# Kernel tuning notes

Hardware: AMD Instinct MI355X
Metric: run time of the kernel (lower is better)

Reference implementation:

```python
import jax, jax.numpy as jnp
import numpy as np

B, H, S, D = 2, 16, 2048, 64  # batch, heads, seq_len, depth (F_hidden)
EPS_ADJ = 1e-09
NEG_INF = -1000000000.0


def iswiglu(x):
    # x * silu(x) == x^2 * sigmoid(x), always >= 0
    return x * jax.nn.silu(x)


def setup_inputs() -> dict:
    key = jax.random.key(0)
    ks = jax.random.split(key, 8)
    Hin = jax.random.normal(ks[0], (B, H, S, D), jnp.float32)
    Hk = jax.random.normal(ks[1], (B, H, S, D), jnp.float32)
    Hv = jax.random.normal(ks[2], (B, H, S, D), jnp.float32)
    A = jax.random.normal(ks[3], (B, H, D, D), jnp.float32)
    # causal (look-ahead) mask: 1 where attention is disallowed
    mask = jnp.triu(jnp.ones((S, S), jnp.float32), k=1)[None, None, :, :]
    xavier = np.sqrt(2.0 / (D + D)).astype(np.float32)  # xavier_normal gain=1 for [D,D] fans
    W = jax.random.normal(ks[4], (H, D, D), jnp.float32) * xavier
    pw = jax.random.normal(ks[5], (H, D, D), jnp.float32) * xavier
    a = jax.random.normal(ks[6], (H, D, D), jnp.float32) * xavier
    b = jnp.zeros((H, D, D), jnp.float32)
    ba = jnp.zeros((H, D, D), jnp.float32)
    return {"Hin": Hin, "Hk": Hk, "Hv": Hv, "A": A, "mask": mask,
            "W": W, "b": b, "pw": pw, "a": a, "ba": ba}


def reference(Hin, Hk, Hv, A, mask, W, b, pw, a, ba):
    # metric-tensor transform: AW = iSwiGLU(W @ A + b) + eps   [B,H,D,D]
    x = jnp.einsum('hij,bhjk->bhik', W, A) + b[None]
    AW = iswiglu(x) + EPS_ADJ
    # energy-curvature tensor: avAp = a @ AW**pw + ba           [B,H,D,D]
    Ap = jnp.power(AW, pw[None])
    avAp = jnp.einsum('hij,bhjk->bhik', a, Ap) + ba[None]
    # bilinear attention scores: (Hin @ avAp) @ Hk^T / sqrt(D)  [B,H,S,S]
    q = jnp.matmul(Hin, avAp)
    Ep = jnp.matmul(q, jnp.swapaxes(Hk, -1, -2)) / jnp.sqrt(jnp.float32(D))
    E = jax.nn.softmax(Ep + mask * NEG_INF, axis=-1)
    Hout = jnp.matmul(E, Hv)                                   # [B,H,S,D]
    return Hout
```

## Files before the change

kernel.cpp:

```cpp
#include <hip/hip_runtime.h>


typedef short v8s __attribute__((ext_vector_type(8)));
typedef float v4f __attribute__((ext_vector_type(4)));

__device__ __forceinline__ float bf2f(unsigned short u) {
    union { unsigned int i; float f; } v; v.i = ((unsigned int)u) << 16; return v.f;
}
__device__ __forceinline__ unsigned short f2bf(float f) {
    unsigned int u = __float_as_uint(f);
    u += 0x7fffu + ((u >> 16) & 1u);
    return (unsigned short)(u >> 16);
}
__device__ __forceinline__ v4f mfma16(v8s a, v8s b, v4f c) {
    return __builtin_amdgcn_mfma_f32_16x16x32_bf16(a, b, c, 0, 0, 0);
}
__device__ __forceinline__ void gload_lds16(const void* g, void* l) {
    __builtin_amdgcn_global_load_lds(
        (const __attribute__((address_space(1))) void*)g,
        (__attribute__((address_space(3))) void*)l, 16, 0, 0);
}
__device__ __forceinline__ void block_sync() {
    asm volatile("" ::: "memory");
    __builtin_amdgcn_s_barrier();
    asm volatile("" ::: "memory");
}
__device__ __forceinline__ float fexp2(float x) {
    float r;
    asm volatile("v_exp_f32 %0, %1" : "=v"(r) : "v"(x));
    return r;
}

__global__ __launch_bounds__(256)
void pre1_kernel(const float* __restrict__ A,  const float* __restrict__ W,
                 const float* __restrict__ b,  const float* __restrict__ pw,
                 float* __restrict__ Pbuf)
{
    __shared__ float sA[4096], sW[512];
    const int bx = blockIdx.x, bh = blockIdx.y, h = bh & 15, t = threadIdx.x;
    const int lcol = t & 63, lrow = t >> 6, r0 = bx * 8;
    for (int i = t; i < 4096; i += 256) sA[i] = A[bh*4096 + i];
    for (int i = t; i < 512;  i += 256) sW[i] = W[h*4096 + r0*64 + i];
    __syncthreads();
    double acc[2];
    #pragma unroll
    for (int e = 0; e < 2; ++e)
        acc[e] = (double)b[h*4096 + (r0 + lrow + 4*e)*64 + lcol];
    #pragma unroll 4
    for (int jj = 0; jj < 16; ++jj) {
        double a0 = (double)sA[(4*jj+0)*64 + lcol];
        double a1 = (double)sA[(4*jj+1)*64 + lcol];
        double a2 = (double)sA[(4*jj+2)*64 + lcol];
        double a3 = (double)sA[(4*jj+3)*64 + lcol];
        #pragma unroll
        for (int e = 0; e < 2; ++e) {
            const float* wr = &sW[(lrow + 4*e)*64 + 4*jj];
            acc[e] += (double)wr[0]*a0 + (double)wr[1]*a1
                    + (double)wr[2]*a2 + (double)wr[3]*a3;
        }
    }
    #pragma unroll
    for (int e = 0; e < 2; ++e) {
        int idx = (r0 + lrow + 4*e)*64 + lcol;
        double v = acc[e];
        double sig = 1.0 / (1.0 + exp(-v));
        Pbuf[bh*4096 + idx] = (float)pow(v*v*sig + 1e-9, (double)pw[h*4096 + idx]);
    }
}

__global__ __launch_bounds__(256)
void pre2_kernel(const float* __restrict__ a,  const float* __restrict__ ba,
                 const float* __restrict__ Pbuf, float* __restrict__ avap)
{
    __shared__ float sP[4096], sa[512];
    const int bx = blockIdx.x, bh = blockIdx.y, h = bh & 15, t = threadIdx.x;
    const int lcol = t & 63, lrow = t >> 6, r0 = bx * 8;
    for (int i = t; i < 4096; i += 256) sP[i] = Pbuf[bh*4096 + i];
    for (int i = t; i < 512;  i += 256) sa[i] = a[h*4096 + r0*64 + i];
    __syncthreads();
    double acc[2];
    #pragma unroll
    for (int e = 0; e < 2; ++e)
        acc[e] = (double)ba[h*4096 + (r0 + lrow + 4*e)*64 + lcol];
    #pragma unroll 4
    for (int jj = 0; jj < 16; ++jj) {
        double a0 = (double)sP[(4*jj+0)*64 + lcol];
        double a1 = (double)sP[(4*jj+1)*64 + lcol];
        double a2 = (double)sP[(4*jj+2)*64 + lcol];
        double a3 = (double)sP[(4*jj+3)*64 + lcol];
        #pragma unroll
        for (int e = 0; e < 2; ++e) {
            const float* wr = &sa[(lrow + 4*e)*64 + 4*jj];
            acc[e] += (double)wr[0]*a0 + (double)wr[1]*a1
                    + (double)wr[2]*a2 + (double)wr[3]*a3;
        }
    }
    #pragma unroll
    for (int e = 0; e < 2; ++e)
        avap[bh*4096 + (r0 + lrow + 4*e)*64 + lcol] = (float)acc[e];
}

__global__ __launch_bounds__(256)
void pre_legacy(const float* __restrict__ A,  const float* __restrict__ W,
                const float* __restrict__ b,  const float* __restrict__ pw,
                const float* __restrict__ a,  const float* __restrict__ ba,
                float* __restrict__ avap)
{
    __shared__ float sW[4096], sA[4096], sP[4096];
    const int bh = blockIdx.x, h = bh & 15, t = threadIdx.x;
    const int lcol = t & 63, lrow = t >> 6;
    for (int i = t; i < 4096; i += 256) { sW[i] = W[h*4096+i]; sA[i] = A[bh*4096+i]; }
    __syncthreads();
    {
        double acc[16];
        #pragma unroll
        for (int e = 0; e < 16; ++e)
            acc[e] = (double)b[h*4096 + (lrow + 4*e)*64 + lcol];
        #pragma unroll 4
        for (int jj = 0; jj < 16; ++jj) {
            double a0 = (double)sA[(4*jj+0)*64 + lcol];
            double a1 = (double)sA[(4*jj+1)*64 + lcol];
            double a2 = (double)sA[(4*jj+2)*64 + lcol];
            double a3 = (double)sA[(4*jj+3)*64 + lcol];
            #pragma unroll
            for (int e = 0; e < 16; ++e) {
                const float* wr = &sW[(lrow + 4*e)*64 + 4*jj];
                acc[e] += (double)wr[0]*a0 + (double)wr[1]*a1
                        + (double)wr[2]*a2 + (double)wr[3]*a3;
            }
        }
        #pragma unroll
        for (int e = 0; e < 16; ++e) {
            int idx = (lrow + 4*e)*64 + lcol;
            double v = acc[e];
            double sig = 1.0 / (1.0 + exp(-v));
            sP[idx] = (float)pow(v*v*sig + 1e-9, (double)pw[h*4096 + idx]);
        }
    }
    __syncthreads();
    for (int i = t; i < 4096; i += 256) sW[i] = a[h*4096+i];
    __syncthreads();
    {
        double acc[16];
        #pragma unroll
        for (int e = 0; e < 16; ++e)
            acc[e] = (double)ba[h*4096 + (lrow + 4*e)*64 + lcol];
        #pragma unroll 4
        for (int jj = 0; jj < 16; ++jj) {
            double a0 = (double)sP[(4*jj+0)*64 + lcol];
            double a1 = (double)sP[(4*jj+1)*64 + lcol];
            double a2 = (double)sP[(4*jj+2)*64 + lcol];
            double a3 = (double)sP[(4*jj+3)*64 + lcol];
            #pragma unroll
            for (int e = 0; e < 16; ++e) {
                const float* wr = &sW[(lrow + 4*e)*64 + 4*jj];
                acc[e] += (double)wr[0]*a0 + (double)wr[1]*a1
                        + (double)wr[2]*a2 + (double)wr[3]*a3;
            }
        }
        #pragma unroll
        for (int e = 0; e < 16; ++e)
            avap[bh*4096 + (lrow + 4*e)*64 + lcol] = (float)acc[e];
    }
}

__global__ __launch_bounds__(256)
void q_kernel(const float* __restrict__ Hin, const float* __restrict__ avap,
              float* __restrict__ qout)
{
    __shared__ float sH[4096], sAv[4096];
    const int qt = blockIdx.x, bh = blockIdx.y, t = threadIdx.x;
    const int lcol = t & 63, lrow = t >> 6;
    const int base = bh*131072 + qt*4096;
    for (int i = t; i < 4096; i += 256) { sH[i] = Hin[base+i]; sAv[i] = avap[bh*4096+i]; }
    __syncthreads();
    float acc[16];
    #pragma unroll
    for (int e = 0; e < 16; ++e) acc[e] = 0.0f;
    #pragma unroll 4
    for (int jj = 0; jj < 16; ++jj) {
        float a0 = sAv[(4*jj+0)*64 + lcol];
        float a1 = sAv[(4*jj+1)*64 + lcol];
        float a2 = sAv[(4*jj+2)*64 + lcol];
        float a3 = sAv[(4*jj+3)*64 + lcol];
        #pragma unroll
        for (int e = 0; e < 16; ++e) {
            const float* hr = &sH[(lrow + 4*e)*64 + 4*jj];
            acc[e] += hr[0]*a0 + hr[1]*a1 + hr[2]*a2 + hr[3]*a3;
        }
    }
    #pragma unroll
    for (int e = 0; e < 16; ++e)
        qout[base + (lrow + 4*e)*64 + lcol] = acc[e] * 0.125f;
}

__global__ __launch_bounds__(256)
void kvprep_kernel(const float* __restrict__ Hk, const float* __restrict__ Hv,
                   unsigned short* __restrict__ kv)
{
    __shared__ float sV[4096];
    const int kt = blockIdx.x, bh = blockIdx.y, t = threadIdx.x;
    const float* hk = Hk + bh*131072 + kt*4096;
    const float* hv = Hv + bh*131072 + kt*4096;
    unsigned short* dst = kv + (size_t)(bh*32 + kt) * 12288;

    #pragma unroll
    for (int it = 0; it < 2; ++it) {
        int item = t + 256*it;
        int kr = item >> 3, oc = item & 7;
        const float* src = hk + kr*64 + oc*8;
        float4 g0 = *(const float4*)(src);
        float4 g1 = *(const float4*)(src + 4);
        float fv[8] = {g0.x,g0.y,g0.z,g0.w,g1.x,g1.y,g1.z,g1.w};
        v8s hi, lo;
        #pragma unroll
        for (int j = 0; j < 8; ++j) {
            unsigned short h = f2bf(fv[j]);
            hi[j] = (short)h;
            lo[j] = (short)f2bf(fv[j] - bf2f(h));
        }
        int addr = kr*64 + ((oc ^ (kr & 7)) << 3);
        *(v8s*)(dst + addr) = hi;
        *(v8s*)(dst + 4096 + addr) = lo;
    }
    #pragma unroll
    for (int i = 0; i < 4; ++i) {
        int idx = t + 256*i;
        int kr = idx >> 4, d0 = (idx & 15) * 4;
        float4 g = *(const float4*)(hv + kr*64 + d0);
        float gv[4] = {g.x, g.y, g.z, g.w};
        #pragma unroll
        for (int j = 0; j < 4; ++j)
            sV[kr*64 + ((d0 + j + kr) & 63)] = gv[j];
    }
    __syncthreads();
    #pragma unroll
    for (int it = 0; it < 2; ++it) {
        int item = t + 256*it;
        int d = item >> 3, oc = item & 7;
        v8s o;
        #pragma unroll
        for (int j = 0; j < 8; ++j) {
            int kr = oc*8 + j;
            o[j] = (short)f2bf(sV[kr*64 + ((d + kr) & 63)]);
        }
        *(v8s*)(dst + 8192 + d*64 + ((oc ^ (d & 7)) << 3)) = o;
    }
}

#define TILE_HW 12288
#define PBASE   24576
#define QLO     8192
#define AVT     16384

__global__ __launch_bounds__(512, 4)
void attn_kernel(const unsigned short* __restrict__ kv,
                 const float* __restrict__ Hin,
                 const float* __restrict__ avap,
                 float* __restrict__ io)
{
    __shared__ __align__(16) unsigned short sm16[32768];
    const int t    = threadIdx.x;
    const int w    = t >> 6;
    const int wq   = w & 3;
    const int lane = t & 63;
    const int l15  = lane & 15;
    const int quad = lane >> 4;
    const int g    = (blockIdx.x & 7) * 64 + (blockIdx.x >> 3);
    const int bh   = g >> 4;
    const int x    = g & 15;
    const int bhb  = bh * 131072;
    const int qt_a = x, qt_b = 31 - x;
    const int qsel = (w < 4) ? qt_a : qt_b;
    const int q0   = qsel * 64;
    const char* kvb = (const char*)(kv + (size_t)bh * 32 * TILE_HW);
    const int sl   = (quad ^ (l15 & 7)) << 3;
    const int wrow0 = (w < 4) ? wq*16 : 64 + wq*16;

    #pragma unroll
    for (int i = 0; i < 16; ++i) {
        int p = t + 512*i;
        int r = p >> 6, c = p & 63;
        int grow = (r < 64) ? (qt_a*64 + r) : (qt_b*64 + (r - 64));
        float v = Hin[bhb + grow*64 + c];
        unsigned short h = f2bf(v);
        int ad = r*64 + ((((c >> 3) ^ (r & 7)) << 3) | (c & 7));
        sm16[ad] = h;
        sm16[QLO + ad] = f2bf(v - bf2f(h));
    }
    #pragma unroll
    for (int i = 0; i < 8; ++i) {
        int p = t + 512*i;
        int k = p >> 6, n = p & 63;
        float v = avap[bh*4096 + p];
        unsigned short h = f2bf(v);
        int ad = n*64 + ((((k >> 3) ^ (n & 7)) << 3) | (k & 7));
        sm16[AVT + ad] = h;
        sm16[AVT + 4096 + ad] = f2bf(v - bf2f(h));
    }
    asm volatile("s_waitcnt lgkmcnt(0)" ::: "memory");
    block_sync();

    v4f qacc[4];
    {
        const int aoff = (wrow0 + l15)*64 + sl;
        v8s ahi0 = *(const v8s*)&sm16[aoff];
        v8s ahi1 = *(const v8s*)&sm16[aoff ^ 32];
        v8s alo0 = *(const v8s*)&sm16[QLO + aoff];
        v8s alo1 = *(const v8s*)&sm16[QLO + (aoff ^ 32)];
        #pragma unroll
        for (int nt = 0; nt < 4; ++nt) {
            const int bo = (16*nt + l15)*64 + sl;
            v8s bhi0 = *(const v8s*)&sm16[AVT + bo];
            v8s bhi1 = *(const v8s*)&sm16[AVT + (bo ^ 32)];
            v8s blo0 = *(const v8s*)&sm16[AVT + 4096 + bo];
            v8s blo1 = *(const v8s*)&sm16[AVT + 4096 + (bo ^ 32)];
            v4f acc = (v4f){0,0,0,0};
            acc = mfma16(alo0, bhi0, acc);
            acc = mfma16(alo1, bhi1, acc);
            acc = mfma16(ahi0, blo0, acc);
            acc = mfma16(ahi1, blo1, acc);
            acc = mfma16(ahi0, bhi0, acc);
            acc = mfma16(ahi1, bhi1, acc);
            qacc[nt] = acc;
        }
    }
    #pragma unroll
    for (int nt = 0; nt < 4; ++nt)
        #pragma unroll
        for (int reg = 0; reg < 4; ++reg) {
            float v = qacc[nt][reg] * 0.1803368801111244f;
            int row = wrow0 + quad*4 + reg;
            int col = 16*nt + l15;
            int ad = row*64 + ((((col >> 3) ^ (row & 7)) << 3) | (col & 7));
            unsigned short h = f2bf(v);
            sm16[ad] = h;
            sm16[QLO + ad] = f2bf(v - bf2f(h));
        }
    asm volatile("s_waitcnt lgkmcnt(0)" ::: "memory");
    v8s qhi[2], qlo[2];
    {
        const int aoff = (wrow0 + l15)*64 + sl;
        qhi[0] = *(const v8s*)&sm16[aoff];
        qhi[1] = *(const v8s*)&sm16[aoff ^ 32];
        qlo[0] = *(const v8s*)&sm16[QLO + aoff];
        qlo[1] = *(const v8s*)&sm16[QLO + (aoff ^ 32)];
    }
    asm volatile("s_waitcnt lgkmcnt(0)" ::: "memory");
    block_sync();

    #pragma unroll
    for (int j = 0; j < 3; ++j) {
        int c = 3*w + j;
        gload_lds16(kvb + c*1024 + (size_t)lane*16, (char*)sm16 + c*1024);
    }

    v4f O[4];
    float m_[4], l_[4];
    #pragma unroll
    for (int i = 0; i < 4; ++i) { O[i] = (v4f){0,0,0,0}; m_[i] = -1e30f; l_[i] = 0.0f; }

    for (int kt = 0; kt <= qt_b; ++kt) {
        const int base = (kt & 1) * TILE_HW;
        if (kt < qt_b) {
            const char* gs = kvb + (size_t)(kt+1) * (TILE_HW*2);
            char* lb = (char*)sm16 + ((kt+1) & 1) * (TILE_HW*2);
            #pragma unroll
            for (int j = 0; j < 3; ++j) {
                int c = 3*w + j;
                gload_lds16(gs + c*1024 + (size_t)lane*16, lb + c*1024);
            }
            asm volatile("s_waitcnt vmcnt(3)" ::: "memory");
        } else {
            asm volatile("s_waitcnt vmcnt(0)" ::: "memory");
        }
        block_sync();

        if (kt <= qsel) {
            v4f s[4];
            #pragma unroll
            for (int ct = 0; ct < 4; ++ct) {
                const int kb = base + (16*ct + l15)*64 + sl;
                v8s kh0 = *(const v8s*)&sm16[kb];
                v8s kh1 = *(const v8s*)&sm16[kb ^ 32];
                v8s kl0 = *(const v8s*)&sm16[kb + 4096];
                v8s kl1 = *(const v8s*)&sm16[(kb ^ 32) + 4096];
                v4f a = (v4f){0,0,0,0};
                a = mfma16(qlo[0], kh0, a);
                a = mfma16(qlo[1], kh1, a);
                a = mfma16(qhi[0], kl0, a);
                a = mfma16(qhi[1], kl1, a);
                a = mfma16(qhi[0], kh0, a);
                a = mfma16(qhi[1], kh1, a);
                s[ct] = a;
            }

            if (kt == qsel) {
                #pragma unroll
                for (int ct = 0; ct < 4; ++ct)
                    #pragma unroll
                    for (int r = 0; r < 4; ++r)
                        if (16*ct + l15 > 16*wq + quad*4 + r) s[ct][r] = -1e30f;
            }

            float pv[4][4];
            #pragma unroll
            for (int reg = 0; reg < 4; ++reg) {
                float rm = fmaxf(fmaxf(s[0][reg], s[1][reg]), fmaxf(s[2][reg], s[3][reg]));
                rm = fmaxf(rm, __shfl_xor(rm, 1));
                rm = fmaxf(rm, __shfl_xor(rm, 2));
                rm = fmaxf(rm, __shfl_xor(rm, 4));
                rm = fmaxf(rm, __shfl_xor(rm, 8));
                float mn = fmaxf(m_[reg], rm);
                float al = fexp2(m_[reg] - mn);
                m_[reg] = mn;
                float rs = 0.0f;
                #pragma unroll
                for (int ct = 0; ct < 4; ++ct) {
                    float e = fexp2(s[ct][reg] - mn);
                    pv[ct][reg] = e; rs += e;
                }
                rs += __shfl_xor(rs, 1);
                rs += __shfl_xor(rs, 2);
                rs += __shfl_xor(rs, 4);
                rs += __shfl_xor(rs, 8);
                l_[reg] = l_[reg]*al + rs;
                #pragma unroll
                for (int d = 0; d < 4; ++d) O[d][reg] *= al;
            }

            #pragma unroll
            for (int reg = 0; reg < 4; ++reg) {
                const int row = quad*4 + reg;
                #pragma unroll
                for (int ct = 0; ct < 4; ++ct)
                    sm16[PBASE + w*1024 + row*64 +
                         ((((2*ct + (l15 >> 3)) ^ (row & 7)) << 3) | (l15 & 7))]
                        = f2bf(pv[ct][reg]);
            }
            asm volatile("s_waitcnt lgkmcnt(0)" ::: "memory");

            const int pb = PBASE + w*1024 + l15*64 + sl;
            v8s pA0 = *(const v8s*)&sm16[pb];
            v8s pA1 = *(const v8s*)&sm16[pb ^ 32];
            #pragma unroll
            for (int d = 0; d < 4; ++d) {
                const int vb = base + 8192 + (16*d + l15)*64 + sl;
                v8s v0 = *(const v8s*)&sm16[vb];
                v8s v1 = *(const v8s*)&sm16[vb ^ 32];
                O[d] = mfma16(pA0, v0, O[d]);
                O[d] = mfma16(pA1, v1, O[d]);
            }
        }
        asm volatile("s_waitcnt lgkmcnt(0)" ::: "memory");
        block_sync();
    }

    #pragma unroll
    for (int reg = 0; reg < 4; ++reg) {
        float inv = 1.0f / l_[reg];
        int row = q0 + 16*wq + quad*4 + reg;
        #pragma unroll
        for (int d = 0; d < 4; ++d)
            io[bhb + row*64 + 16*d + l15] = O[d][reg] * inv;
    }
}

#define KHI 0
#define KLO 4608
#define VTB 9216
#define PB  13824

__global__ __launch_bounds__(256, 4)
void attn_legacy(const float* __restrict__ Hk, const float* __restrict__ Hv,
                 float* __restrict__ io)
{
    __shared__ __align__(16) unsigned short sm16[18432];
    const int t    = threadIdx.x;
    const int w    = t >> 6;
    const int lane = t & 63;
    const int l15  = lane & 15;
    const int quad = lane >> 4;
    const int x    = blockIdx.x;
    const int bh   = blockIdx.y;
    const int bhb  = bh * 131072;

    for (int pass = 0; pass < 2; ++pass) {
        const int qt = pass ? (31 - x) : x;
        const int q0 = qt * 64;

        v8s qhi[2], qlo[2];
        {
            const float* qr = io + bhb + (q0 + 16*w + l15)*64 + quad*8;
            #pragma unroll
            for (int ks = 0; ks < 2; ++ks)
                #pragma unroll
                for (int j = 0; j < 8; ++j) {
                    float qv = qr[32*ks + j];
                    unsigned short h = f2bf(qv);
                    unsigned short l = f2bf(qv - bf2f(h));
                    qhi[ks][j] = (short)h; qlo[ks][j] = (short)l;
                }
        }

        v4f O[4];
        float m_[4], l_[4];
        #pragma unroll
        for (int i = 0; i < 4; ++i) { O[i] = (v4f){0,0,0,0}; m_[i] = -1e30f; l_[i] = 0.0f; }

        for (int kt = 0; kt <= qt; ++kt) {
            __syncthreads();
            const int tb = bhb + kt*4096;
            #pragma unroll 4
            for (int i = 0; i < 16; ++i) {
                int p = t + 256*i;
                int kr = p >> 6, d = p & 63;
                float kvv = Hk[tb + p];
                unsigned short h = f2bf(kvv);
                sm16[KHI + kr*72 + d] = h;
                sm16[KLO + kr*72 + d] = f2bf(kvv - bf2f(h));
                sm16[VTB + d*72 + kr] = f2bf(Hv[tb + p]);
            }
            __syncthreads();

            v4f s[4];
            #pragma unroll
            for (int ct = 0; ct < 4; ++ct) {
                const unsigned short* kb = &sm16[(16*ct + l15)*72 + quad*8];
                v8s kh0 = *(const v8s*)(kb + KHI);
                v8s kh1 = *(const v8s*)(kb + KHI + 32);
                v8s kl0 = *(const v8s*)(kb + KLO);
                v8s kl1 = *(const v8s*)(kb + KLO + 32);
                v4f a = (v4f){0,0,0,0};
                a = mfma16(qlo[0], kh0, a);
                a = mfma16(qlo[1], kh1, a);
                a = mfma16(qhi[0], kl0, a);
                a = mfma16(qhi[1], kl1, a);
                a = mfma16(qhi[0], kh0, a);
                a = mfma16(qhi[1], kh1, a);
                s[ct] = a;
            }

            if (kt == qt) {
                #pragma unroll
                for (int ct = 0; ct < 4; ++ct)
                    #pragma unroll
                    for (int r = 0; r < 4; ++r)
                        if (16*ct + l15 > 16*w + quad*4 + r) s[ct][r] = -1e30f;
            }

            float pv[4][4];
            #pragma unroll
            for (int reg = 0; reg < 4; ++reg) {
                float rm = fmaxf(fmaxf(s[0][reg], s[1][reg]), fmaxf(s[2][reg], s[3][reg]));
                rm = fmaxf(rm, __shfl_xor(rm, 1));
                rm = fmaxf(rm, __shfl_xor(rm, 2));
                rm = fmaxf(rm, __shfl_xor(rm, 4));
                rm = fmaxf(rm, __shfl_xor(rm, 8));
                float mn = fmaxf(m_[reg], rm);
                float al = __expf(m_[reg] - mn);
                m_[reg] = mn;
                float rs = 0.0f;
                #pragma unroll
                for (int ct = 0; ct < 4; ++ct) {
                    float e = __expf(s[ct][reg] - mn);
                    pv[ct][reg] = e; rs += e;
                }
                rs += __shfl_xor(rs, 1);
                rs += __shfl_xor(rs, 2);
                rs += __shfl_xor(rs, 4);
                rs += __shfl_xor(rs, 8);
                l_[reg] = l_[reg]*al + rs;
                #pragma unroll
                for (int d = 0; d < 4; ++d) O[d][reg] *= al;
            }

            #pragma unroll
            for (int reg = 0; reg < 4; ++reg)
                #pragma unroll
                for (int ct = 0; ct < 4; ++ct)
                    sm16[PB + w*1152 + (quad*4+reg)*72 + 16*ct + l15] = f2bf(pv[ct][reg]);
            asm volatile("s_waitcnt lgkmcnt(0)" ::: "memory");

            const unsigned short* pb = &sm16[PB + w*1152 + l15*72 + quad*8];
            v8s pA0 = *(const v8s*)(pb);
            v8s pA1 = *(const v8s*)(pb + 32);
            #pragma unroll
            for (int d = 0; d < 4; ++d) {
                const unsigned short* vb = &sm16[VTB + (16*d + l15)*72 + quad*8];
                v8s v0 = *(const v8s*)(vb);
                v8s v1 = *(const v8s*)(vb + 32);
                O[d] = mfma16(pA0, v0, O[d]);
                O[d] = mfma16(pA1, v1, O[d]);
            }
        }

        #pragma unroll
        for (int reg = 0; reg < 4; ++reg) {
            float inv = 1.0f / l_[reg];
            int row = q0 + 16*w + quad*4 + reg;
            #pragma unroll
            for (int d = 0; d < 4; ++d)
                io[bhb + row*64 + 16*d + l15] = O[d][reg] * inv;
        }
        __syncthreads();
    }
}

extern "C" void kernel_launch(void* const* d_in, const int* in_sizes, int n_in,
                              void* d_out, int out_size, void* d_ws, size_t ws_size,
                              hipStream_t stream)
{
    const float* Hin = (const float*)d_in[0];
    const float* Hk  = (const float*)d_in[1];
    const float* Hv  = (const float*)d_in[2];
    const float* A   = (const float*)d_in[3];
    const float* W   = (const float*)d_in[5];
    const float* b   = (const float*)d_in[6];
    const float* pw  = (const float*)d_in[7];
    const float* a   = (const float*)d_in[8];
    const float* ba  = (const float*)d_in[9];
    float* out  = (float*)d_out;
    float* avap = (float*)d_ws;

    const size_t KVOFF = 1u << 20;
    const size_t NEED  = KVOFF + (size_t)1024 * 24576;

    if (ws_size >= NEED) {
        float* Pbuf = (float*)((char*)d_ws + (512u << 10));
        unsigned short* kvb = (unsigned short*)((char*)d_ws + KVOFF);
        pre1_kernel<<<dim3(8, 32), dim3(256), 0, stream>>>(A, W, b, pw, Pbuf);
        pre2_kernel<<<dim3(8, 32), dim3(256), 0, stream>>>(a, ba, Pbuf, avap);
        kvprep_kernel<<<dim3(32, 32), dim3(256), 0, stream>>>(Hk, Hv, kvb);
        attn_kernel<<<dim3(512), dim3(512), 0, stream>>>(kvb, Hin, avap, out);
    } else {
        pre_legacy<<<dim3(32), dim3(256), 0, stream>>>(A, W, b, pw, a, ba, avap);
        q_kernel<<<dim3(32, 32), dim3(256), 0, stream>>>(Hin, avap, out);
        attn_legacy<<<dim3(16, 32), dim3(256), 0, stream>>>(Hk, Hv, out);
    }
}
```

Before: 206.3 us.

## Fuse prep kernels and move a@P matmul into attention kernel via MFMA

Merges the K/V bf16 split prep and the first metric-transform stage into one launch by dispatching on block index, and drops the separate pre2 kernel. The attention kernel now computes avAp = a @ P + ba itself with split-bf16 MFMAs in shared memory before forming q. The first stage also switches from double precision to float with fast exp/log2-based pow. Launch count falls from four to two and the double-precision ALU work goes away, at the cost of redundant per-block a@P work and some precision risk from the float pow.

```diff
diff --git a/kernel.cpp b/kernel.cpp
--- a/kernel.cpp
+++ b/kernel.cpp
@@ -32,72 +32,97 @@
 }
 
 __global__ __launch_bounds__(256)
-void pre1_kernel(const float* __restrict__ A,  const float* __restrict__ W,
+void prep_kernel(const float* __restrict__ Hk, const float* __restrict__ Hv,
+                 unsigned short* __restrict__ kv,
+                 const float* __restrict__ A,  const float* __restrict__ W,
                  const float* __restrict__ b,  const float* __restrict__ pw,
                  float* __restrict__ Pbuf)
 {
-    __shared__ float sA[4096], sW[512];
-    const int bx = blockIdx.x, bh = blockIdx.y, h = bh & 15, t = threadIdx.x;
-    const int lcol = t & 63, lrow = t >> 6, r0 = bx * 8;
-    for (int i = t; i < 4096; i += 256) sA[i] = A[bh*4096 + i];
-    for (int i = t; i < 512;  i += 256) sW[i] = W[h*4096 + r0*64 + i];
-    __syncthreads();
-    double acc[2];
-    #pragma unroll
-    for (int e = 0; e < 2; ++e)
-        acc[e] = (double)b[h*4096 + (r0 + lrow + 4*e)*64 + lcol];
-    #pragma unroll 4
-    for (int jj = 0; jj < 16; ++jj) {
-        double a0 = (double)sA[(4*jj+0)*64 + lcol];
-        double a1 = (double)sA[(4*jj+1)*64 + lcol];
-        double a2 = (double)sA[(4*jj+2)*64 + lcol];
-        double a3 = (double)sA[(4*jj+3)*64 + lcol];
+    __shared__ __align__(16) float smem[4608];
+    const int blk = blockIdx.x, t = threadIdx.x;
+
+    if (blk < 1024) {
+        const int kt = blk & 31, bh = blk >> 5;
+        float* sV = smem;
+        const float* hk = Hk + bh*131072 + kt*4096;
+        const float* hv = Hv + bh*131072 + kt*4096;
+        unsigned short* dst = kv + (size_t)(bh*32 + kt) * 12288;
+
+        #pragma unroll
+        for (int it = 0; it < 2; ++it) {
+            int item = t + 256*it;
+            int kr = item >> 3, oc = item & 7;
+            const float* src = hk + kr*64 + oc*8;
+            float4 g0 = *(const float4*)(src);
+            float4 g1 = *(const float4*)(src + 4);
+            float fv[8] = {g0.x,g0.y,g0.z,g0.w,g1.x,g1.y,g1.z,g1.w};
+            v8s hi, lo;
+            #pragma unroll
+            for (int j = 0; j < 8; ++j) {
+                unsigned short h = f2bf(fv[j]);
+                hi[j] = (short)h;
+                lo[j] = (short)f2bf(fv[j] - bf2f(h));
+            }
+            int addr = kr*64 + ((oc ^ (kr & 7)) << 3);
+            *(v8s*)(dst + addr) = hi;
+            *(v8s*)(dst + 4096 + addr) = lo;
+        }
+        #pragma unroll
+        for (int i = 0; i < 4; ++i) {
+            int idx = t + 256*i;
+            int kr = idx >> 4, d0 = (idx & 15) * 4;
+            float4 g = *(const float4*)(hv + kr*64 + d0);
+            float gv[4] = {g.x, g.y, g.z, g.w};
+            #pragma unroll
+            for (int j = 0; j < 4; ++j)
+                sV[kr*64 + ((d0 + j + kr) & 63)] = gv[j];
+        }
+        __syncthreads();
+        #pragma unroll
+        for (int it = 0; it < 2; ++it) {
+            int item = t + 256*it;
+            int d = item >> 3, oc = item & 7;
+            v8s o;
+            #pragma unroll
+            for (int j = 0; j < 8; ++j) {
+                int kr = oc*8 + j;
+                o[j] = (short)f2bf(sV[kr*64 + ((d + kr) & 63)]);
+            }
+            *(v8s*)(dst + 8192 + d*64 + ((oc ^ (d & 7)) << 3)) = o;
+        }
+    } else {
+        const int i2 = blk - 1024, bx = i2 & 7, bh = i2 >> 3, h = bh & 15;
+        const int lcol = t & 63, lrow = t >> 6, r0 = bx * 8;
+        float* sA = smem;
+        float* sW = smem + 4096;
+        for (int i = t; i < 4096; i += 256) sA[i] = A[bh*4096 + i];
+        for (int i = t; i < 512;  i += 256) sW[i] = W[h*4096 + r0*64 + i];
+        __syncthreads();
+        float acc[2];
+        #pragma unroll
+        for (int e = 0; e < 2; ++e)
+            acc[e] = b[h*4096 + (r0 + lrow + 4*e)*64 + lcol];
+        #pragma unroll 4
+        for (int jj = 0; jj < 16; ++jj) {
+            float a0 = sA[(4*jj+0)*64 + lcol];
+            float a1 = sA[(4*jj+1)*64 + lcol];
+            float a2 = sA[(4*jj+2)*64 + lcol];
+            float a3 = sA[(4*jj+3)*64 + lcol];
+            #pragma unroll
+            for (int e = 0; e < 2; ++e) {
+                const float* wr = &sW[(lrow + 4*e)*64 + 4*jj];
+                acc[e] += wr[0]*a0 + wr[1]*a1 + wr[2]*a2 + wr[3]*a3;
+            }
+        }
         #pragma unroll
         for (int e = 0; e < 2; ++e) {
-            const float* wr = &sW[(lrow + 4*e)*64 + 4*jj];
-            acc[e] += (double)wr[0]*a0 + (double)wr[1]*a1
-                    + (double)wr[2]*a2 + (double)wr[3]*a3;
-        }
-    }
-    #pragma unroll
-    for (int e = 0; e < 2; ++e) {
-        int idx = (r0 + lrow + 4*e)*64 + lcol;
-        double v = acc[e];
-        double sig = 1.0 / (1.0 + exp(-v));
-        Pbuf[bh*4096 + idx] = (float)pow(v*v*sig + 1e-9, (double)pw[h*4096 + idx]);
-    }
-}
-
-__global__ __launch_bounds__(256)
-void pre2_kernel(const float* __restrict__ a,  const float* __restrict__ ba,
-                 const float* __restrict__ Pbuf, float* __restrict__ avap)
-{
-    __shared__ float sP[4096], sa[512];
-    const int bx = blockIdx.x, bh = blockIdx.y, h = bh & 15, t = threadIdx.x;
-    const int lcol = t & 63, lrow = t >> 6, r0 = bx * 8;
-    for (int i = t; i < 4096; i += 256) sP[i] = Pbuf[bh*4096 + i];
-    for (int i = t; i < 512;  i += 256) sa[i] = a[h*4096 + r0*64 + i];
-    __syncthreads();
-    double acc[2];
-    #pragma unroll
-    for (int e = 0; e < 2; ++e)
-        acc[e] = (double)ba[h*4096 + (r0 + lrow + 4*e)*64 + lcol];
-    #pragma unroll 4
-    for (int jj = 0; jj < 16; ++jj) {
-        double a0 = (double)sP[(4*jj+0)*64 + lcol];
-        double a1 = (double)sP[(4*jj+1)*64 + lcol];
-        double a2 = (double)sP[(4*jj+2)*64 + lcol];
-        double a3 = (double)sP[(4*jj+3)*64 + lcol];
-        #pragma unroll
-        for (int e = 0; e < 2; ++e) {
-            const float* wr = &sa[(lrow + 4*e)*64 + 4*jj];
-            acc[e] += (double)wr[0]*a0 + (double)wr[1]*a1
-                    + (double)wr[2]*a2 + (double)wr[3]*a3;
-        }
-    }
-    #pragma unroll
-    for (int e = 0; e < 2; ++e)
-        avap[bh*4096 + (r0 + lrow + 4*e)*64 + lcol] = (float)acc[e];
+            int idx = (r0 + lrow + 4*e)*64 + lcol;
+            float v = acc[e];
+            float sig = 1.0f / (1.0f + __expf(-v));
+            float aw = v*v*sig + 1e-9f;
+            Pbuf[bh*4096 + idx] = exp2f(pw[h*4096 + idx] * log2f(aw));
+        }
+    }
 }
 
 __global__ __launch_bounds__(256)
@@ -194,69 +219,18 @@
         qout[base + (lrow + 4*e)*64 + lcol] = acc[e] * 0.125f;
 }
 
-__global__ __launch_bounds__(256)
-void kvprep_kernel(const float* __restrict__ Hk, const float* __restrict__ Hv,
-                   unsigned short* __restrict__ kv)
-{
-    __shared__ float sV[4096];
-    const int kt = blockIdx.x, bh = blockIdx.y, t = threadIdx.x;
-    const float* hk = Hk + bh*131072 + kt*4096;
-    const float* hv = Hv + bh*131072 + kt*4096;
-    unsigned short* dst = kv + (size_t)(bh*32 + kt) * 12288;
-
-    #pragma unroll
-    for (int it = 0; it < 2; ++it) {
-        int item = t + 256*it;
-        int kr = item >> 3, oc = item & 7;
-        const float* src = hk + kr*64 + oc*8;
-        float4 g0 = *(const float4*)(src);
-        float4 g1 = *(const float4*)(src + 4);
-        float fv[8] = {g0.x,g0.y,g0.z,g0.w,g1.x,g1.y,g1.z,g1.w};
-        v8s hi, lo;
-        #pragma unroll
-        for (int j = 0; j < 8; ++j) {
-            unsigned short h = f2bf(fv[j]);
-            hi[j] = (short)h;
-            lo[j] = (short)f2bf(fv[j] - bf2f(h));
-        }
-        int addr = kr*64 + ((oc ^ (kr & 7)) << 3);
-        *(v8s*)(dst + addr) = hi;
-        *(v8s*)(dst + 4096 + addr) = lo;
-    }
-    #pragma unroll
-    for (int i = 0; i < 4; ++i) {
-        int idx = t + 256*i;
-        int kr = idx >> 4, d0 = (idx & 15) * 4;
-        float4 g = *(const float4*)(hv + kr*64 + d0);
-        float gv[4] = {g.x, g.y, g.z, g.w};
-        #pragma unroll
-        for (int j = 0; j < 4; ++j)
-            sV[kr*64 + ((d0 + j + kr) & 63)] = gv[j];
-    }
-    __syncthreads();
-    #pragma unroll
-    for (int it = 0; it < 2; ++it) {
-        int item = t + 256*it;
-        int d = item >> 3, oc = item & 7;
-        v8s o;
-        #pragma unroll
-        for (int j = 0; j < 8; ++j) {
-            int kr = oc*8 + j;
-            o[j] = (short)f2bf(sV[kr*64 + ((d + kr) & 63)]);
-        }
-        *(v8s*)(dst + 8192 + d*64 + ((oc ^ (d & 7)) << 3)) = o;
-    }
-}
-
 #define TILE_HW 12288
 #define PBASE   24576
 #define QLO     8192
 #define AVT     16384
+#define AH      24576
 
 __global__ __launch_bounds__(512, 4)
 void attn_kernel(const unsigned short* __restrict__ kv,
                  const float* __restrict__ Hin,
-                 const float* __restrict__ avap,
+                 const float* __restrict__ Pbuf,
+                 const float* __restrict__ ag,
+                 const float* __restrict__ bag,
                  float* __restrict__ io)
 {
     __shared__ __align__(16) unsigned short sm16[32768];
@@ -268,6 +242,7 @@
     const int quad = lane >> 4;
     const int g    = (blockIdx.x & 7) * 64 + (blockIdx.x >> 3);
     const int bh   = g >> 4;
+    const int h    = bh & 15;
     const int x    = g & 15;
     const int bhb  = bh * 131072;
     const int qt_a = x, qt_b = 31 - x;
@@ -283,20 +258,75 @@
         int r = p >> 6, c = p & 63;
         int grow = (r < 64) ? (qt_a*64 + r) : (qt_b*64 + (r - 64));
         float v = Hin[bhb + grow*64 + c];
-        unsigned short h = f2bf(v);
+        unsigned short hv_ = f2bf(v);
         int ad = r*64 + ((((c >> 3) ^ (r & 7)) << 3) | (c & 7));
-        sm16[ad] = h;
-        sm16[QLO + ad] = f2bf(v - bf2f(h));
+        sm16[ad] = hv_;
+        sm16[QLO + ad] = f2bf(v - bf2f(hv_));
     }
     #pragma unroll
     for (int i = 0; i < 8; ++i) {
         int p = t + 512*i;
-        int k = p >> 6, n = p & 63;
-        float v = avap[bh*4096 + p];
-        unsigned short h = f2bf(v);
-        int ad = n*64 + ((((k >> 3) ^ (n & 7)) << 3) | (k & 7));
-        sm16[AVT + ad] = h;
-        sm16[AVT + 4096 + ad] = f2bf(v - bf2f(h));
+        int j = p >> 6, n = p & 63;
+        float v = Pbuf[bh*4096 + p];
+        unsigned short hv_ = f2bf(v);
+        int ad = n*64 + ((((j >> 3) ^ (n & 7)) << 3) | (j & 7));
+        sm16[AVT + ad] = hv_;
+        sm16[AVT + 4096 + ad] = f2bf(v - bf2f(hv_));
+    }
+    #pragma unroll
+    for (int i = 0; i < 8; ++i) {
+        int p = t + 512*i;
+        int r = p >> 6, c = p & 63;
+        float v = ag[h*4096 + p];
+        unsigned short hv_ = f2bf(v);
+        int ad = r*64 + ((((c >> 3) ^ (r & 7)) << 3) | (c & 7));
+        sm16[AH + ad] = hv_;
+        sm16[AH + 4096 + ad] = f2bf(v - bf2f(hv_));
+    }
+    asm volatile("s_waitcnt lgkmcnt(0)" ::: "memory");
+    block_sync();
+
+    v4f av[4];
+    {
+        const int aoff = AH + (16*wq + l15)*64 + sl;
+        v8s ahi0 = *(const v8s*)&sm16[aoff];
+        v8s ahi1 = *(const v8s*)&sm16[aoff ^ 32];
+        v8s alo0 = *(const v8s*)&sm16[aoff + 4096];
+        v8s alo1 = *(const v8s*)&sm16[(aoff ^ 32) + 4096];
+        #pragma unroll
+        for (int nt = 0; nt < 4; ++nt) {
+            const int bo = AVT + (16*nt + l15)*64 + sl;
+            v8s bhi0 = *(const v8s*)&sm16[bo];
+            v8s bhi1 = *(const v8s*)&sm16[bo ^ 32];
+            v8s blo0 = *(const v8s*)&sm16[bo + 4096];
+            v8s blo1 = *(const v8s*)&sm16[(bo ^ 32) + 4096];
+            v4f acc = (v4f){0,0,0,0};
+            acc = mfma16(alo0, bhi0, acc);
+            acc = mfma16(alo1, bhi1, acc);
+            acc = mfma16(ahi0, blo0, acc);
+            acc = mfma16(ahi1, blo1, acc);
+            acc = mfma16(ahi0, bhi0, acc);
+            acc = mfma16(ahi1, bhi1, acc);
+            #pragma unroll
+            for (int reg = 0; reg < 4; ++reg)
+                acc[reg] += bag[h*4096 + (16*wq + quad*4 + reg)*64 + 16*nt + l15];
+            av[nt] = acc;
+        }
+    }
+    block_sync();
+    if (w < 4) {
+        #pragma unroll
+        for (int nt = 0; nt < 4; ++nt)
+            #pragma unroll
+            for (int reg = 0; reg < 4; ++reg) {
+                float v = av[nt][reg];
+                int kk = 16*wq + quad*4 + reg;
+                int n  = 16*nt + l15;
+                int ad = n*64 + ((((kk >> 3) ^ (n & 7)) << 3) | (kk & 7));
+                unsigned short hv_ = f2bf(v);
+                sm16[AVT + ad] = hv_;
+                sm16[AVT + 4096 + ad] = f2bf(v - bf2f(hv_));
+            }
     }
     asm volatile("s_waitcnt lgkmcnt(0)" ::: "memory");
     block_sync();
@@ -310,11 +340,11 @@
         v8s alo1 = *(const v8s*)&sm16[QLO + (aoff ^ 32)];
         #pragma unroll
         for (int nt = 0; nt < 4; ++nt) {
-            const int bo = (16*nt + l15)*64 + sl;
-            v8s bhi0 = *(const v8s*)&sm16[AVT + bo];
-            v8s bhi1 = *(const v8s*)&sm16[AVT + (bo ^ 32)];
-            v8s blo0 = *(const v8s*)&sm16[AVT + 4096 + bo];
-            v8s blo1 = *(const v8s*)&sm16[AVT + 4096 + (bo ^ 32)];
+            const int bo = AVT + (16*nt + l15)*64 + sl;
+            v8s bhi0 = *(const v8s*)&sm16[bo];
+            v8s bhi1 = *(const v8s*)&sm16[bo ^ 32];
+            v8s blo0 = *(const v8s*)&sm16[bo + 4096];
+            v8s blo1 = *(const v8s*)&sm16[(bo ^ 32) + 4096];
             v4f acc = (v4f){0,0,0,0};
             acc = mfma16(alo0, bhi0, acc);
             acc = mfma16(alo1, bhi1, acc);
@@ -333,9 +363,9 @@
             int row = wrow0 + quad*4 + reg;
             int col = 16*nt + l15;
             int ad = row*64 + ((((col >> 3) ^ (row & 7)) << 3) | (col & 7));
-            unsigned short h = f2bf(v);
-            sm16[ad] = h;
-            sm16[QLO + ad] = f2bf(v - bf2f(h));
+            unsigned short hv_ = f2bf(v);
+            sm16[ad] = hv_;
+            sm16[QLO + ad] = f2bf(v - bf2f(hv_));
         }
     asm volatile("s_waitcnt lgkmcnt(0)" ::: "memory");
     v8s qhi[2], qlo[2];
@@ -621,19 +651,19 @@
     const float* a   = (const float*)d_in[8];
     const float* ba  = (const float*)d_in[9];
     float* out  = (float*)d_out;
-    float* avap = (float*)d_ws;
 
     const size_t KVOFF = 1u << 20;
     const size_t NEED  = KVOFF + (size_t)1024 * 24576;
 
     if (ws_size >= NEED) {
-        float* Pbuf = (float*)((char*)d_ws + (512u << 10));
+        float* Pbuf = (float*)d_ws;
         unsigned short* kvb = (unsigned short*)((char*)d_ws + KVOFF);
-        pre1_kernel<<<dim3(8, 32), dim3(256), 0, stream>>>(A, W, b, pw, Pbuf);
-        pre2_kernel<<<dim3(8, 32), dim3(256), 0, stream>>>(a, ba, Pbuf, avap);
-        kvprep_kernel<<<dim3(32, 32), dim3(256), 0, stream>>>(Hk, Hv, kvb);
-        attn_kernel<<<dim3(512), dim3(512), 0, stream>>>(kvb, Hin, avap, out);
+        prep_kernel<<<dim3(1280), dim3(256), 0, stream>>>(Hk, Hv, kvb,
+                                                          A, W, b, pw, Pbuf);
+        attn_kernel<<<dim3(512), dim3(512), 0, stream>>>(kvb, Hin, Pbuf,
+                                                         a, ba, out);
     } else {
+        float* avap = (float*)d_ws;
         pre_legacy<<<dim3(32), dim3(256), 0, stream>>>(A, W, b, pw, a, ba, avap);
         q_kernel<<<dim3(32, 32), dim3(256), 0, stream>>>(Hin, avap, out);
         attn_legacy<<<dim3(16, 32), dim3(256), 0, stream>>>(Hk, Hv, out);
```

Result: faster. 198.9 us (-3.6%).
